# Kernel optimization log

Measured on AMD Instinct MI355X. Metric: run time of the kernel, lower is better.

The kernel has to match this reference:

```python
import jax, jax.numpy as jnp
import numpy as np

# dims
N, E, Z, C, NB = 8192, 131072, 10, 128, 8
R_MAX, P_CUT, AVG_NEIGH = 5.0, 5, 16.0
SH_DIM, N_L, N_LAYERS, MLP_H = 16, 4, 2, 16
# which l each of the 16 sh components belongs to
L_OF_M = jnp.array([0, 1, 1, 1, 2, 2, 2, 2, 2, 3, 3, 3, 3, 3, 3, 3])


def spherical_harmonics(u):
    """Real spherical harmonics up to l=3, e3nn 'component' normalization. u: [E,3] unit vectors."""
    x, y, z = u[:, 0], u[:, 1], u[:, 2]
    x2, y2, z2 = x * x, y * y, z * z
    s3, s5, s15 = np.sqrt(3.0), np.sqrt(5.0), np.sqrt(15.0)
    a33, a32, a31, a30 = 0.25 * np.sqrt(70.0), np.sqrt(105.0), 0.25 * np.sqrt(42.0), 0.5 * np.sqrt(7.0)
    Y = [jnp.ones_like(x),
         s3 * x, s3 * y, s3 * z,
         s15 * x * y, s15 * y * z, 0.5 * s5 * (3 * z2 - 1.0), s15 * x * z, 0.5 * s15 * (x2 - y2),
         a33 * y * (3 * x2 - y2), a32 * x * y * z, a31 * y * (5 * z2 - 1.0),
         a30 * z * (5 * z2 - 3.0), a31 * x * (5 * z2 - 1.0), 0.5 * a32 * z * (x2 - y2),
         a33 * x * (x2 - 3 * y2)]
    return jnp.stack(Y, axis=-1)  # [E,16]


def radial_embedding(r):
    """Bessel radial basis with smooth polynomial cutoff (p=5). r: [E] edge lengths."""
    x = r / R_MAX
    p = float(P_CUT)
    cut = (1.0 - 0.5 * (p + 1.0) * (p + 2.0) * x ** P_CUT
           + p * (p + 2.0) * x ** (P_CUT + 1) - 0.5 * p * (p + 1.0) * x ** (P_CUT + 2))
    cut = jnp.where(x < 1.0, cut, 0.0)
    n = jnp.arange(1, NB + 1, dtype=r.dtype)
    bessel = np.sqrt(2.0 / R_MAX) * jnp.sin(n[None, :] * jnp.pi * x[:, None]) / r[:, None]
    return bessel * cut[:, None]  # [E,8]


def _forward(positions, node_attrs, shifts, W_embed, W_up, R_w1, R_w2, R_w3,
             W_out, w_sc, w_prod, W_plin, w_ro0, ro_w1, ro_w2, edge_index):
    sender, receiver = edge_index[0], edge_index[1]
    vec = positions[receiver] - positions[sender] + shifts          # [E,3]
    lengths = jnp.linalg.norm(vec, axis=-1) + 1e-9                  # [E]
    sh = spherical_harmonics(vec / lengths[:, None])                # [E,16]
    edge_feats = radial_embedding(lengths)                          # [E,8]

    # node embedding: scalars into l=0 slot of [N,C,16]
    scalars = node_attrs @ W_embed                                  # [N,C]
    feats = jnp.zeros((N, C, SH_DIM), scalars.dtype).at[:, :, 0].set(scalars)

    outputs = []
    for L in range(N_LAYERS):
        # linear up (channel mixing, per irrep component)
        h = jnp.einsum('ncm,cd->ndm', feats, W_up[L])               # [N,C,16]
        # radial MLP -> per-edge, per-channel, per-l tensor-product weights
        r = jax.nn.silu(edge_feats @ R_w1[L])
        r = jax.nn.silu(r @ R_w2[L])
        w = (r @ R_w3[L]).reshape(E, C, N_L)                        # [E,C,4]
        w_m = jnp.take(w, L_OF_M, axis=2)                           # [E,C,16]
        # channel-wise tensor product: scalar node feat x SH, scatter to receiver
        msg = h[sender, :, 0][:, :, None] * w_m * sh[:, None, :]    # [E,C,16]
        agg = jax.ops.segment_sum(msg, receiver, num_segments=N) / AVG_NEIGH
        m = jnp.einsum('ncm,cd->ndm', agg, W_out[L])                # [N,C,16]
        # element-dependent skip connection
        sc = h * (node_attrs @ w_sc[L])[:, :, None]
        # product basis (correlation 3): element-weighted powers of scalar part
        s = m[:, :, 0]                                              # [N,C]
        coeff = jnp.einsum('nz,zck->nck', node_attrs, w_prod[L])    # [N,C,3]
        powers = jnp.stack([jnp.ones_like(s), s, s * s], axis=-1)   # [N,C,3]
        scale = jnp.sum(coeff * powers, axis=-1)                    # [N,C]
        feats = jnp.einsum('ncm,cd->ndm', m * scale[:, :, None], W_plin[L]) + sc
        if L == 0:
            outputs.append(feats[:, :, 0] @ w_ro0)                  # linear readout [N]
        else:
            outputs.append(jax.nn.silu(feats[:, :, 0] @ ro_w1) @ ro_w2)  # nonlinear readout [N]
    return outputs[0] + outputs[1]


def setup_inputs() -> dict:
    key = jax.random.key(0)
    ks = jax.random.split(key, 16)
    positions = jax.random.normal(ks[0], (N, 3), jnp.float32) * 1.5
    elems = jax.random.randint(ks[1], (N,), 0, Z)
    node_attrs = jax.nn.one_hot(elems, Z, dtype=jnp.float32)
    edge_index = jax.random.randint(ks[2], (2, E), 0, N)
    shifts = jnp.zeros((E, 3), jnp.float32)
    g = lambda k, sh, fan: jax.random.normal(k, sh, jnp.float32) / np.sqrt(fan)
    return {
        'positions': positions, 'node_attrs': node_attrs, 'shifts': shifts,
        'W_embed': g(ks[3], (Z, C), Z),
        'W_up': g(ks[4], (N_LAYERS, C, C), C),
        'R_w1': g(ks[5], (N_LAYERS, NB, 64), NB),
        'R_w2': g(ks[6], (N_LAYERS, 64, 64), 64),
        'R_w3': g(ks[7], (N_LAYERS, 64, C * N_L), 64),
        'W_out': g(ks[8], (N_LAYERS, C, C), C),
        'w_sc': g(ks[9], (N_LAYERS, Z, C), 1),
        'w_prod': g(ks[10], (N_LAYERS, Z, C, 3), 1) * 0.1,
        'W_plin': g(ks[11], (N_LAYERS, C, C), C),
        'w_ro0': g(ks[12], (C,), C),
        'ro_w1': g(ks[13], (C, MLP_H), C),
        'ro_w2': g(ks[14], (MLP_H,), MLP_H),
        'edge_index': edge_index,
    }


def reference(positions, node_attrs, shifts, W_embed, W_up, R_w1, R_w2, R_w3,
              W_out, w_sc, w_prod, W_plin, w_ro0, ro_w1, ro_w2, edge_index):
    return _forward(positions, node_attrs, shifts, W_embed, W_up, R_w1, R_w2, R_w3,
                    W_out, w_sc, w_prod, W_plin, w_ro0, ro_w1, ro_w2, edge_index)
```

## Files before the change

kernel.cpp:

```cpp
#include <hip/hip_runtime.h>
#include <math.h>

constexpr int kN = 8192;
constexpr int kE = 131072;
constexpr int NPB = 16;

typedef short bf16x8 __attribute__((ext_vector_type(8)));
typedef float f32x4 __attribute__((ext_vector_type(4)));
typedef unsigned short ushort_t;
typedef unsigned int uint_t;

__device__ __forceinline__ float silu_f(float x) { return x / (1.f + __expf(-x)); }

__device__ __forceinline__ ushort_t f2b(float f) {
  uint_t x = __float_as_uint(f);
  uint_t r = (x + 0x7fffu + ((x >> 16) & 1u)) >> 16;
  return (ushort_t)r;
}
__device__ __forceinline__ float b2f(ushort_t u) {
  return __uint_as_float(((uint_t)u) << 16);
}

__global__ __launch_bounds__(256) void zero_ints_kernel(int* __restrict__ a, int* __restrict__ b) {
  int i = blockIdx.x * 256 + threadIdx.x;
  if (i < kN) { a[i] = 0; b[i] = 0; }
}

__global__ __launch_bounds__(256) void elem_kernel(const float* __restrict__ attrs, int* __restrict__ elem) {
  int n = blockIdx.x * 256 + threadIdx.x;
  if (n >= kN) return;
  const float* a = attrs + (size_t)n * 10;
  int best = 0; float bv = a[0];
  #pragma unroll
  for (int z = 1; z < 10; ++z) { float v = a[z]; if (v > bv) { bv = v; best = z; } }
  elem[n] = best;
}

__global__ __launch_bounds__(256) void init_feats_kernel(const float* __restrict__ W_embed,
                                                         const int* __restrict__ elem,
                                                         ushort_t* __restrict__ F) {
  int i = blockIdx.x * 256 + threadIdx.x;
  int n = i >> 7, c = i & 127;
  F[(size_t)n * 2048 + c] = f2b(W_embed[(size_t)elem[n] * 128 + c]);
}

__global__ __launch_bounds__(256) void count_kernel(const int* __restrict__ ei, int* __restrict__ counts) {
  int e = blockIdx.x * 256 + threadIdx.x;
  if (e < kE) atomicAdd(&counts[ei[kE + e]], 1);
}

__global__ __launch_bounds__(1024) void scan_kernel(const int* __restrict__ counts, int* __restrict__ offs) {
  __shared__ int tmp[1024];
  int t = threadIdx.x;
  int loc[8]; int s = 0;
  #pragma unroll
  for (int i = 0; i < 8; ++i) { loc[i] = s; s += counts[t*8 + i]; }
  tmp[t] = s;
  __syncthreads();
  for (int d = 1; d < 1024; d <<= 1) {
    int v = (t >= d) ? tmp[t - d] : 0;
    __syncthreads();
    tmp[t] += v;
    __syncthreads();
  }
  int pre = (t == 0) ? 0 : tmp[t - 1];
  #pragma unroll
  for (int i = 0; i < 8; ++i) offs[t*8 + i] = pre + loc[i];
  if (t == 1023) offs[kN] = tmp[1023];
}

__global__ __launch_bounds__(256) void fill_kernel(const int* __restrict__ ei, const int* __restrict__ offs,
                                                   int* __restrict__ cursor, int* __restrict__ eids,
                                                   int* __restrict__ sends) {
  int e = blockIdx.x * 256 + threadIdx.x;
  if (e >= kE) return;
  int s = ei[e];
  int r = ei[kE + e];
  int pos = atomicAdd(&cursor[r], 1);
  eids[offs[r] + pos] = e;
  sends[offs[r] + pos] = s;
}

__global__ __launch_bounds__(256) void geom_kernel(const float* __restrict__ pos,
                                                   const float* __restrict__ shifts,
                                                   const int* __restrict__ ei,
                                                   const int* __restrict__ eids,
                                                   const int* __restrict__ sends,
                                                   float* __restrict__ sh,
                                                   float* __restrict__ rb) {
  int slot = blockIdx.x * 256 + threadIdx.x;
  if (slot >= kE) return;
  int e = eids[slot];
  int s = sends[slot];
  int r = ei[kE + e];
  float vx = pos[r*3+0] - pos[s*3+0] + shifts[(size_t)e*3+0];
  float vy = pos[r*3+1] - pos[s*3+1] + shifts[(size_t)e*3+1];
  float vz = pos[r*3+2] - pos[s*3+2] + shifts[(size_t)e*3+2];
  float len = sqrtf(vx*vx + vy*vy + vz*vz) + 1e-9f;
  float inv = 1.f / len;
  float x = vx*inv, y = vy*inv, z = vz*inv;
  float x2 = x*x, y2 = y*y, z2 = z*z;
  const float s3  = 1.7320508075688772f;
  const float s5  = 2.2360679774997896f;
  const float s15 = 3.8729833462074170f;
  const float a33 = 2.0916500663351889f;
  const float a32 = 10.246950765959598f;
  const float a31 = 1.6201851746019651f;
  const float a30 = 1.3228756555322954f;
  float4* shp = (float4*)(sh + (size_t)slot * 16);
  shp[0] = make_float4(1.f, s3*x, s3*y, s3*z);
  shp[1] = make_float4(s15*x*y, s15*y*z, 0.5f*s5*(3.f*z2 - 1.f), s15*x*z);
  shp[2] = make_float4(0.5f*s15*(x2 - y2), a33*y*(3.f*x2 - y2), a32*x*y*z, a31*y*(5.f*z2 - 1.f));
  shp[3] = make_float4(a30*z*(5.f*z2 - 3.f), a31*x*(5.f*z2 - 1.f), 0.5f*a32*z*(x2 - y2), a33*x*(x2 - 3.f*y2));
  float xr = len * 0.2f;
  float cut = 0.f;
  if (xr < 1.f) {
    float x5 = xr*xr*xr*xr*xr;
    cut = 1.f - 21.f*x5 + 35.f*x5*xr - 15.f*x5*xr*xr;
  }
  float pref = 0.63245553203367587f * cut * inv;
  const float PI = 3.14159265358979323846f;
  float theta = PI * xr;
  float sn, cs;
  __sincosf(theta, &sn, &cs);
  float twoc = 2.f * cs;
  float b[8];
  float s_prev = 0.f, s_cur = sn;
  b[0] = pref * s_cur;
  #pragma unroll
  for (int k = 1; k < 8; ++k) {
    float s_next = twoc * s_cur - s_prev;
    s_prev = s_cur; s_cur = s_next;
    b[k] = pref * s_cur;
  }
  float4* rbp = (float4*)(rb + (size_t)slot * 8);
  rbp[0] = make_float4(b[0], b[1], b[2], b[3]);
  rbp[1] = make_float4(b[4], b[5], b[6], b[7]);
}

__global__ __launch_bounds__(256) void radial_kernel(const float* __restrict__ rb,
                                                     const float* __restrict__ W1,
                                                     const float* __restrict__ W2,
                                                     ushort_t* __restrict__ r2) {
  __shared__ float rbs[128][8];
  __shared__ float W1s[8*64];
  __shared__ ushort_t B2s[64][72];
  __shared__ ushort_t r1s[128][72];
  const int tid = threadIdx.x;
  const size_t ebase = (size_t)blockIdx.x * 128;
  {
    int r = tid >> 1, q = tid & 1;
    *(float4*)&rbs[r][q*4] = *(const float4*)&rb[(ebase + r)*8 + q*4];
  }
  for (int i = tid; i < 512; i += 256) W1s[i] = W1[i];
  for (int i = tid; i < 4096; i += 256) {
    int k = i >> 6, col = i & 63;
    B2s[col][k] = f2b(W2[i]);
  }
  __syncthreads();
  {
    int col = tid & 63;
    int r0 = (tid >> 6) * 32;
    #pragma unroll 4
    for (int rr = 0; rr < 32; ++rr) {
      int row = r0 + rr;
      float v = 0.f;
      #pragma unroll
      for (int i = 0; i < 8; ++i) v = fmaf(rbs[row][i], W1s[i*64 + col], v);
      r1s[row][col] = f2b(silu_f(v));
    }
  }
  __syncthreads();
  const int lane = tid & 63, wv = tid >> 6;
  const int wr = wv * 32;
  const int fr = lane & 15, kg = (lane >> 4) * 8;
  f32x4 acc[2][4] = {};
  #pragma unroll
  for (int ks = 0; ks < 2; ++ks) {
    const int k0 = ks*32 + kg;
    bf16x8 af[2], bfr[4];
    #pragma unroll
    for (int i = 0; i < 2; ++i) af[i] = *(const bf16x8*)&r1s[wr + i*16 + fr][k0];
    #pragma unroll
    for (int j = 0; j < 4; ++j) bfr[j] = *(const bf16x8*)&B2s[j*16 + fr][k0];
    #pragma unroll
    for (int i = 0; i < 2; ++i)
      #pragma unroll
      for (int j = 0; j < 4; ++j)
        acc[i][j] = __builtin_amdgcn_mfma_f32_16x16x32_bf16(af[i], bfr[j], acc[i][j], 0, 0, 0);
  }
  __syncthreads();
  const int dcol = lane & 15, drow4 = (lane >> 4) * 4;
  #pragma unroll
  for (int i = 0; i < 2; ++i)
    #pragma unroll
    for (int j = 0; j < 4; ++j)
      #pragma unroll
      for (int r = 0; r < 4; ++r) {
        int row = wr + i*16 + drow4 + r;
        int col = j*16 + dcol;
        r1s[row][col] = f2b(silu_f(acc[i][j][r]));
      }
  __syncthreads();
  for (int idx = tid * 8; idx < 128*64; idx += 256*8) {
    int r = idx >> 6, k = idx & 63;
    *(int4*)&r2[(ebase + r)*64 + k] = *(const int4*)&r1s[r][k];
  }
}

__global__ __launch_bounds__(256) void transpose_w_kernel(const float* __restrict__ W, ushort_t* __restrict__ WT) {
  int i = blockIdx.x * 256 + threadIdx.x;
  int d = i >> 7, c = i & 127;
  WT[i] = f2b(W[c*128 + d]);
}

__global__ __launch_bounds__(256) void transpose_r3_kernel(const float* __restrict__ R3, ushort_t* __restrict__ R3T) {
  int i = blockIdx.x * 256 + threadIdx.x;
  int t = i >> 6, j = i & 63;
  int c = t & 127, l = t >> 7;
  R3T[i] = f2b(R3[j*512 + c*4 + l]);
}

template<bool SCALED, bool EPI, bool L0>
__global__ __launch_bounds__(256) void mgemm_kernel(
    const ushort_t* __restrict__ A, size_t aStride,
    const ushort_t* __restrict__ BT,
    ushort_t* __restrict__ O, size_t oStride,
    const float* __restrict__ scaleBuf,
    const ushort_t* __restrict__ Hbuf,
    const float* __restrict__ wscL,
    const int* __restrict__ elem)
{
  __shared__ ushort_t As[128][136];
  __shared__ ushort_t Bs[128][136];
  const int tid = threadIdx.x;
  const size_t rowbase = (size_t)blockIdx.x * 128;

  for (int idx = tid * 8; idx < 128 * 128; idx += 256 * 8) {
    int r = idx >> 7, k = idx & 127;
    *(int4*)&Bs[r][k] = *(const int4*)&BT[(size_t)r * 128 + k];
  }
  for (int idx = tid * 8; idx < 128 * 128; idx += 256 * 8) {
    int r = idx >> 7, k = idx & 127;
    size_t grow = rowbase + r;
    const ushort_t* ap = A + grow * aStride + k;
    if (SCALED) {
      const float* sp = scaleBuf + (grow >> 4) * 128 + k;
      uint_t u[4];
      #pragma unroll
      for (int q = 0; q < 4; ++q) {
        ushort_t lo = f2b(b2f(ap[2*q])   * sp[2*q]);
        ushort_t hi = f2b(b2f(ap[2*q+1]) * sp[2*q+1]);
        u[q] = (uint_t)lo | ((uint_t)hi << 16);
      }
      *(int4*)&As[r][k] = make_int4((int)u[0], (int)u[1], (int)u[2], (int)u[3]);
    } else {
      *(int4*)&As[r][k] = *(const int4*)ap;
    }
  }
  __syncthreads();

  const int lane = tid & 63, wv = tid >> 6;
  const int wr = (wv >> 1) * 64, wc = (wv & 1) * 64;
  const int fr = lane & 15;
  const int kg = (lane >> 4) * 8;
  f32x4 acc[4][4] = {};
  #pragma unroll
  for (int ks = 0; ks < 4; ++ks) {
    const int k0 = ks * 32 + kg;
    bf16x8 af[4], bfr[4];
    #pragma unroll
    for (int i = 0; i < 4; ++i) af[i]  = *(const bf16x8*)&As[wr + i*16 + fr][k0];
    #pragma unroll
    for (int j = 0; j < 4; ++j) bfr[j] = *(const bf16x8*)&Bs[wc + j*16 + fr][k0];
    #pragma unroll
    for (int i = 0; i < 4; ++i)
      #pragma unroll
      for (int j = 0; j < 4; ++j)
        acc[i][j] = __builtin_amdgcn_mfma_f32_16x16x32_bf16(af[i], bfr[j], acc[i][j], 0, 0, 0);
  }

  const int dcol = lane & 15, drow4 = (lane >> 4) * 4;
  #pragma unroll
  for (int i = 0; i < 4; ++i) {
    #pragma unroll
    for (int j = 0; j < 4; ++j) {
      int col = wc + j*16 + dcol;
      #pragma unroll
      for (int r = 0; r < 4; ++r) {
        int row = wr + i*16 + drow4 + r;
        size_t grow = rowbase + row;
        float v = acc[i][j][r];
        if (EPI) {
          if (!L0 || ((grow & 15) == 0)) {
            int ee = elem[grow >> 4];
            v += b2f(Hbuf[grow * 128 + col]) * wscL[(size_t)ee * 128 + col];
          }
        }
        O[grow * oStride + col] = f2b(v);
      }
    }
  }
}

__global__ __launch_bounds__(256, 2) void gather_kernel(
    const int* __restrict__ offs, const int* __restrict__ sends,
    const ushort_t* __restrict__ r2csr,
    const float* __restrict__ shcsr,
    const ushort_t* __restrict__ R3T,
    const ushort_t* __restrict__ H,
    ushort_t* __restrict__ AGG)
{
  __shared__ ushort_t r2s[2][32][68];
  __shared__ ushort_t h0s[2][32][68];
  __shared__ float    shs[2][32][17];
  const int tid = threadIdx.x;
  const int lane = tid & 63;
  const int l = tid >> 6;
  const int cbb = blockIdx.y * 64;
  const int mb = l * l, mc = 2 * l + 1;
  const int fr = lane & 15, g = lane >> 4, kg = g * 8;
  const int n0 = blockIdx.x * NPB;
  const int hslot = tid >> 3, hseg = tid & 7;
  const int s0i = tid, s1i = 256 + tid;

  bf16x8 bfrag[4][2];
  #pragma unroll
  for (int j = 0; j < 4; ++j)
    #pragma unroll
    for (int ks = 0; ks < 2; ++ks)
      bfrag[j][ks] = *(const bf16x8*)&R3T[(size_t)(l*128 + cbb + j*16 + fr) * 64 + ks*32 + kg];

  {
    int a0 = offs[n0], a1 = offs[n0 + 1];
    int4 h0v = make_int4(0,0,0,0), r2v = make_int4(0,0,0,0);
    float sv0 = 0.f, sv1 = 0.f;
    if (a0 + hslot < a1) {
      h0v = *(const int4*)&H[(size_t)sends[a0 + hslot] * 2048 + cbb + hseg * 8];
      r2v = *(const int4*)&r2csr[(size_t)(a0 + hslot) * 64 + hseg * 8];
    }
    if (a0 + (s0i >> 4) < a1) sv0 = shcsr[(size_t)(a0 + (s0i >> 4)) * 16 + (s0i & 15)];
    if (a0 + (s1i >> 4) < a1) sv1 = shcsr[(size_t)(a0 + (s1i >> 4)) * 16 + (s1i & 15)];
    *(int4*)&h0s[0][hslot][hseg * 8] = h0v;
    *(int4*)&r2s[0][hslot][hseg * 8] = r2v;
    shs[0][s0i >> 4][s0i & 15] = sv0;
    shs[0][s1i >> 4][s1i & 15] = sv1;
  }
  __syncthreads();

  int p = 0;
  for (int nn = n0; nn < n0 + NPB; ++nn) {
    const int e0n = offs[nn], e1n = offs[nn + 1];
    int4 h0n = make_int4(0,0,0,0), r2n = make_int4(0,0,0,0);
    float sn0 = 0.f, sn1 = 0.f;
    if (nn + 1 < n0 + NPB) {
      int a0 = offs[nn + 1], a1 = offs[nn + 2];
      if (a0 + hslot < a1) {
        h0n = *(const int4*)&H[(size_t)sends[a0 + hslot] * 2048 + cbb + hseg * 8];
        r2n = *(const int4*)&r2csr[(size_t)(a0 + hslot) * 64 + hseg * 8];
      }
      if (a0 + (s0i >> 4) < a1) sn0 = shcsr[(size_t)(a0 + (s0i >> 4)) * 16 + (s0i & 15)];
      if (a0 + (s1i >> 4) < a1) sn1 = shcsr[(size_t)(a0 + (s1i >> 4)) * 16 + (s1i & 15)];
    }

    float agg[7][4] = {};
    auto compute = [&](int pb) {
      f32x4 acc[2][4] = {};
      #pragma unroll
      for (int ks = 0; ks < 2; ++ks) {
        bf16x8 af[2];
        #pragma unroll
        for (int i = 0; i < 2; ++i) af[i] = *(const bf16x8*)&r2s[pb][i*16 + fr][ks*32 + kg];
        #pragma unroll
        for (int i = 0; i < 2; ++i)
          #pragma unroll
          for (int j = 0; j < 4; ++j)
            acc[i][j] = __builtin_amdgcn_mfma_f32_16x16x32_bf16(af[i], bfrag[j][ks], acc[i][j], 0, 0, 0);
      }
      #pragma unroll
      for (int i = 0; i < 2; ++i)
        #pragma unroll
        for (int r = 0; r < 4; ++r) {
          int slot = i*16 + g*4 + r;
          float shr[7];
          #pragma unroll
          for (int mi = 0; mi < 7; ++mi) shr[mi] = shs[pb][slot][mb + mi];
          #pragma unroll
          for (int j = 0; j < 4; ++j) {
            float wh = acc[i][j][r] * b2f(h0s[pb][slot][j*16 + fr]);
            #pragma unroll
            for (int mi = 0; mi < 7; ++mi)
              if (mi < mc) agg[mi][j] = fmaf(wh, shr[mi], agg[mi][j]);
          }
        }
    };
    compute(p);
    for (int base = e0n + 32; base < e1n; base += 32) {
      __syncthreads();
      int4 h0x = make_int4(0,0,0,0), r2x = make_int4(0,0,0,0);
      float sx0 = 0.f, sx1 = 0.f;
      if (base + hslot < e1n) {
        h0x = *(const int4*)&H[(size_t)sends[base + hslot] * 2048 + cbb + hseg * 8];
        r2x = *(const int4*)&r2csr[(size_t)(base + hslot) * 64 + hseg * 8];
      }
      if (base + (s0i >> 4) < e1n) sx0 = shcsr[(size_t)(base + (s0i >> 4)) * 16 + (s0i & 15)];
      if (base + (s1i >> 4) < e1n) sx1 = shcsr[(size_t)(base + (s1i >> 4)) * 16 + (s1i & 15)];
      *(int4*)&h0s[p][hslot][hseg * 8] = h0x;
      *(int4*)&r2s[p][hslot][hseg * 8] = r2x;
      shs[p][s0i >> 4][s0i & 15] = sx0;
      shs[p][s1i >> 4][s1i & 15] = sx1;
      __syncthreads();
      compute(p);
    }
    #pragma unroll
    for (int mi = 0; mi < 7; ++mi) {
      if (mi < mc) {
        #pragma unroll
        for (int j = 0; j < 4; ++j) {
          float v = agg[mi][j];
          v += __shfl_xor(v, 16, 64);
          v += __shfl_xor(v, 32, 64);
          if (lane < 16)
            AGG[(size_t)nn * 2048 + (mb + mi) * 128 + cbb + j * 16 + lane] = f2b(v * 0.0625f);
        }
      }
    }
    *(int4*)&h0s[p ^ 1][hslot][hseg * 8] = h0n;
    *(int4*)&r2s[p ^ 1][hslot][hseg * 8] = r2n;
    shs[p ^ 1][s0i >> 4][s0i & 15] = sn0;
    shs[p ^ 1][s1i >> 4][s1i & 15] = sn1;
    __syncthreads();
    p ^= 1;
  }
}

__global__ __launch_bounds__(256) void scale_kernel(const ushort_t* __restrict__ M,
                                                    const int* __restrict__ elem,
                                                    const float* __restrict__ wprodL,
                                                    float* __restrict__ scale) {
  int i = blockIdx.x * 256 + threadIdx.x;
  int n = i >> 7, c = i & 127;
  float s = b2f(M[(size_t)n * 2048 + c]);
  const float* co = wprodL + ((size_t)elem[n] * 128 + c) * 3;
  scale[i] = co[0] + s * (co[1] + s * co[2]);
}

__global__ __launch_bounds__(64) void readout_kernel(const ushort_t* __restrict__ F,
                                                     const float* __restrict__ ro0,
                                                     const float* __restrict__ ro1,
                                                     const float* __restrict__ ro2,
                                                     float* __restrict__ out, int layer) {
  int n = blockIdx.x; int t = threadIdx.x;
  const ushort_t* fr = F + (size_t)n * 2048;
  float f0 = b2f(fr[t]), f1 = b2f(fr[t + 64]);
  if (layer == 0) {
    float v = f0 * ro0[t] + f1 * ro0[t + 64];
    #pragma unroll
    for (int m = 32; m > 0; m >>= 1) v += __shfl_xor(v, m, 64);
    if (t == 0) out[n] = v;
  } else {
    float acc = 0.f;
    for (int h = 0; h < 16; ++h) {
      float p = f0 * ro1[t*16 + h] + f1 * ro1[(t + 64)*16 + h];
      #pragma unroll
      for (int m = 32; m > 0; m >>= 1) p += __shfl_xor(p, m, 64);
      acc = fmaf(silu_f(p), ro2[h], acc);
    }
    if (t == 0) out[n] += acc;
  }
}

extern "C" void kernel_launch(void* const* d_in, const int* in_sizes, int n_in,
                              void* d_out, int out_size, void* d_ws, size_t ws_size,
                              hipStream_t stream) {
  (void)in_sizes; (void)n_in; (void)out_size;
  const float* positions = (const float*)d_in[0];
  const float* node_attrs= (const float*)d_in[1];
  const float* shifts    = (const float*)d_in[2];
  const float* W_embed   = (const float*)d_in[3];
  const float* W_up      = (const float*)d_in[4];
  const float* R_w1      = (const float*)d_in[5];
  const float* R_w2      = (const float*)d_in[6];
  const float* R_w3      = (const float*)d_in[7];
  const float* W_out     = (const float*)d_in[8];
  const float* w_sc      = (const float*)d_in[9];
  const float* w_prod    = (const float*)d_in[10];
  const float* W_plin    = (const float*)d_in[11];
  const float* w_ro0     = (const float*)d_in[12];
  const float* ro_w1     = (const float*)d_in[13];
  const float* ro_w2     = (const float*)d_in[14];
  const int*   ei        = (const int*)d_in[15];
  float* out = (float*)d_out;

  char* ws_ptr = (char*)d_ws;
  size_t off = 0;
  auto alloc = [&](size_t nbytes) -> void* {
    void* p = ws_ptr + off;
    off += (nbytes + 255) & ~(size_t)255;
    return p;
  };
  const size_t PB = (size_t)kN * 16 * 128 * sizeof(ushort_t);
  ushort_t* P0    = (ushort_t*)alloc(PB);
  ushort_t* P1    = (ushort_t*)alloc(PB);
  ushort_t* P2    = (ushort_t*)alloc(PB);
  float* shcsr    = (float*)alloc((size_t)kE * 16 * 4);
  float* rbcsr    = (float*)alloc((size_t)kE * 8 * 4);
  ushort_t* r2csr = (ushort_t*)alloc((size_t)kE * 64 * 2);
  float* scaleb   = (float*)alloc((size_t)kN * 128 * 4);
  ushort_t* R3T0  = (ushort_t*)alloc(512 * 64 * 2);
  ushort_t* R3T1  = (ushort_t*)alloc(512 * 64 * 2);
  ushort_t* WTu0  = (ushort_t*)alloc(128 * 128 * 2);
  ushort_t* WTu1  = (ushort_t*)alloc(128 * 128 * 2);
  ushort_t* WTo0  = (ushort_t*)alloc(128 * 128 * 2);
  ushort_t* WTo1  = (ushort_t*)alloc(128 * 128 * 2);
  ushort_t* WTp0  = (ushort_t*)alloc(128 * 128 * 2);
  ushort_t* WTp1  = (ushort_t*)alloc(128 * 128 * 2);
  int* elemb  = (int*)alloc(kN * 4);
  int* counts = (int*)alloc(kN * 4);
  int* cursor = (int*)alloc(kN * 4);
  int* offsb  = (int*)alloc((kN + 1) * 4);
  int* eidsb  = (int*)alloc((size_t)kE * 4);
  int* sendsb = (int*)alloc((size_t)kE * 4);
  if (off > ws_size) return;

  zero_ints_kernel<<<kN/256, 256, 0, stream>>>(counts, cursor);
  elem_kernel<<<kN/256, 256, 0, stream>>>(node_attrs, elemb);
  init_feats_kernel<<<(kN*128)/256, 256, 0, stream>>>(W_embed, elemb, P0);
  count_kernel<<<kE/256, 256, 0, stream>>>(ei, counts);
  scan_kernel<<<1, 1024, 0, stream>>>(counts, offsb);
  fill_kernel<<<kE/256, 256, 0, stream>>>(ei, offsb, cursor, eidsb, sendsb);
  geom_kernel<<<kE/256, 256, 0, stream>>>(positions, shifts, ei, eidsb, sendsb, shcsr, rbcsr);
  transpose_w_kernel<<<64, 256, 0, stream>>>(W_up, WTu0);
  transpose_w_kernel<<<64, 256, 0, stream>>>(W_up + 16384, WTu1);
  transpose_w_kernel<<<64, 256, 0, stream>>>(W_out, WTo0);
  transpose_w_kernel<<<64, 256, 0, stream>>>(W_out + 16384, WTo1);
  transpose_w_kernel<<<64, 256, 0, stream>>>(W_plin, WTp0);
  transpose_w_kernel<<<64, 256, 0, stream>>>(W_plin + 16384, WTp1);
  transpose_r3_kernel<<<128, 256, 0, stream>>>(R_w3, R3T0);
  transpose_r3_kernel<<<128, 256, 0, stream>>>(R_w3 + 32768, R3T1);

  radial_kernel<<<kE/128, 256, 0, stream>>>(rbcsr, R_w1, R_w2, r2csr);
  mgemm_kernel<false,false,false><<<kN/128, 256, 0, stream>>>(
      P0, 2048, WTu0, P1, 2048, nullptr, nullptr, nullptr, nullptr);
  gather_kernel<<<dim3(kN/NPB, 2), 256, 0, stream>>>(offsb, sendsb, r2csr, shcsr, R3T0, P1, P2);
  mgemm_kernel<false,false,false><<<(kN*16)/128, 256, 0, stream>>>(
      P2, 128, WTo0, P0, 128, nullptr, nullptr, nullptr, nullptr);
  scale_kernel<<<(kN*128)/256, 256, 0, stream>>>(P0, elemb, w_prod, scaleb);
  mgemm_kernel<true,true,true><<<(kN*16)/128, 256, 0, stream>>>(
      P0, 128, WTp0, P2, 128, scaleb, P1, w_sc, elemb);
  readout_kernel<<<kN, 64, 0, stream>>>(P2, w_ro0, ro_w1, ro_w2, out, 0);

  radial_kernel<<<kE/128, 256, 0, stream>>>(rbcsr, R_w1 + 512, R_w2 + 4096, r2csr);
  mgemm_kernel<false,false,false><<<(kN*16)/128, 256, 0, stream>>>(
      P2, 128, WTu1, P1, 128, nullptr, nullptr, nullptr, nullptr);
  gather_kernel<<<dim3(kN/NPB, 2), 256, 0, stream>>>(offsb, sendsb, r2csr, shcsr, R3T1, P1, P0);
  mgemm_kernel<false,false,false><<<(kN*16)/128, 256, 0, stream>>>(
      P0, 128, WTo1, P2, 128, nullptr, nullptr, nullptr, nullptr);
  scale_kernel<<<(kN*128)/256, 256, 0, stream>>>(P2, elemb, w_prod + 3840, scaleb);
  mgemm_kernel<true,true,false><<<(kN*16)/128, 256, 0, stream>>>(
      P2, 128, WTp1, P0, 128, scaleb, P1, w_sc + 1280, elemb);
  readout_kernel<<<kN, 64, 0, stream>>>(P0, w_ro0, ro_w1, ro_w2, out, 1);
}
```

Measured before the change: 492.4 us.

## Process one node per block in gather kernel, dropping cross-node prefetch

```diff
diff --git a/kernel.cpp b/kernel.cpp
--- a/kernel.cpp
+++ b/kernel.cpp
@@ -3,7 +3,6 @@
 
 constexpr int kN = 8192;
 constexpr int kE = 131072;
-constexpr int NPB = 16;
 
 typedef short bf16x8 __attribute__((ext_vector_type(8)));
 typedef float f32x4 __attribute__((ext_vector_type(4)));
@@ -311,19 +310,21 @@
     const ushort_t* __restrict__ H,
     ushort_t* __restrict__ AGG)
 {
-  __shared__ ushort_t r2s[2][32][68];
-  __shared__ ushort_t h0s[2][32][68];
-  __shared__ float    shs[2][32][17];
+  __shared__ ushort_t r2s[32][68];
+  __shared__ ushort_t h0s[32][68];
+  __shared__ float    shs[32][17];
   const int tid = threadIdx.x;
   const int lane = tid & 63;
   const int l = tid >> 6;
   const int cbb = blockIdx.y * 64;
   const int mb = l * l, mc = 2 * l + 1;
   const int fr = lane & 15, g = lane >> 4, kg = g * 8;
-  const int n0 = blockIdx.x * NPB;
+  const int n = blockIdx.x;
   const int hslot = tid >> 3, hseg = tid & 7;
   const int s0i = tid, s1i = 256 + tid;
 
+  const int e0 = offs[n], e1 = offs[n + 1];
+
   bf16x8 bfrag[4][2];
   #pragma unroll
   for (int j = 0; j < 4; ++j)
@@ -331,106 +332,65 @@
     for (int ks = 0; ks < 2; ++ks)
       bfrag[j][ks] = *(const bf16x8*)&R3T[(size_t)(l*128 + cbb + j*16 + fr) * 64 + ks*32 + kg];
 
-  {
-    int a0 = offs[n0], a1 = offs[n0 + 1];
-    int4 h0v = make_int4(0,0,0,0), r2v = make_int4(0,0,0,0);
-    float sv0 = 0.f, sv1 = 0.f;
-    if (a0 + hslot < a1) {
-      h0v = *(const int4*)&H[(size_t)sends[a0 + hslot] * 2048 + cbb + hseg * 8];
-      r2v = *(const int4*)&r2csr[(size_t)(a0 + hslot) * 64 + hseg * 8];
-    }
-    if (a0 + (s0i >> 4) < a1) sv0 = shcsr[(size_t)(a0 + (s0i >> 4)) * 16 + (s0i & 15)];
-    if (a0 + (s1i >> 4) < a1) sv1 = shcsr[(size_t)(a0 + (s1i >> 4)) * 16 + (s1i & 15)];
-    *(int4*)&h0s[0][hslot][hseg * 8] = h0v;
-    *(int4*)&r2s[0][hslot][hseg * 8] = r2v;
-    shs[0][s0i >> 4][s0i & 15] = sv0;
-    shs[0][s1i >> 4][s1i & 15] = sv1;
-  }
-  __syncthreads();
-
-  int p = 0;
-  for (int nn = n0; nn < n0 + NPB; ++nn) {
-    const int e0n = offs[nn], e1n = offs[nn + 1];
-    int4 h0n = make_int4(0,0,0,0), r2n = make_int4(0,0,0,0);
-    float sn0 = 0.f, sn1 = 0.f;
-    if (nn + 1 < n0 + NPB) {
-      int a0 = offs[nn + 1], a1 = offs[nn + 2];
-      if (a0 + hslot < a1) {
-        h0n = *(const int4*)&H[(size_t)sends[a0 + hslot] * 2048 + cbb + hseg * 8];
-        r2n = *(const int4*)&r2csr[(size_t)(a0 + hslot) * 64 + hseg * 8];
+  float agg[7][4] = {};
+  for (int base = e0; base < e1; base += 32) {
+    if (base != e0) __syncthreads();
+    {
+      int4 h0v = make_int4(0,0,0,0), r2v = make_int4(0,0,0,0);
+      float sv0 = 0.f, sv1 = 0.f;
+      if (base + hslot < e1) {
+        h0v = *(const int4*)&H[(size_t)sends[base + hslot] * 2048 + cbb + hseg * 8];
+        r2v = *(const int4*)&r2csr[(size_t)(base + hslot) * 64 + hseg * 8];
       }
-      if (a0 + (s0i >> 4) < a1) sn0 = shcsr[(size_t)(a0 + (s0i >> 4)) * 16 + (s0i & 15)];
-      if (a0 + (s1i >> 4) < a1) sn1 = shcsr[(size_t)(a0 + (s1i >> 4)) * 16 + (s1i & 15)];
-    }
-
-    float agg[7][4] = {};
-    auto compute = [&](int pb) {
-      f32x4 acc[2][4] = {};
-      #pragma unroll
-      for (int ks = 0; ks < 2; ++ks) {
-        bf16x8 af[2];
-        #pragma unroll
-        for (int i = 0; i < 2; ++i) af[i] = *(const bf16x8*)&r2s[pb][i*16 + fr][ks*32 + kg];
-        #pragma unroll
-        for (int i = 0; i < 2; ++i)
-          #pragma unroll
-          for (int j = 0; j < 4; ++j)
-            acc[i][j] = __builtin_amdgcn_mfma_f32_16x16x32_bf16(af[i], bfrag[j][ks], acc[i][j], 0, 0, 0);
-      }
+      if (base + (s0i >> 4) < e1) sv0 = shcsr[(size_t)(base + (s0i >> 4)) * 16 + (s0i & 15)];
+      if (base + (s1i >> 4) < e1) sv1 = shcsr[(size_t)(base + (s1i >> 4)) * 16 + (s1i & 15)];
+      *(int4*)&h0s[hslot][hseg * 8] = h0v;
+      *(int4*)&r2s[hslot][hseg * 8] = r2v;
+      shs[s0i >> 4][s0i & 15] = sv0;
+      shs[s1i >> 4][s1i & 15] = sv1;
+    }
+    __syncthreads();
+    f32x4 acc[2][4] = {};
+    #pragma unroll
+    for (int ks = 0; ks < 2; ++ks) {
+      bf16x8 af[2];
+      #pragma unroll
+      for (int i = 0; i < 2; ++i) af[i] = *(const bf16x8*)&r2s[i*16 + fr][ks*32 + kg];
       #pragma unroll
       for (int i = 0; i < 2; ++i)
         #pragma unroll
-        for (int r = 0; r < 4; ++r) {
-          int slot = i*16 + g*4 + r;
-          float shr[7];
-          #pragma unroll
-          for (int mi = 0; mi < 7; ++mi) shr[mi] = shs[pb][slot][mb + mi];
-          #pragma unroll
-          for (int j = 0; j < 4; ++j) {
-            float wh = acc[i][j][r] * b2f(h0s[pb][slot][j*16 + fr]);
-            #pragma unroll
-            for (int mi = 0; mi < 7; ++mi)
-              if (mi < mc) agg[mi][j] = fmaf(wh, shr[mi], agg[mi][j]);
-          }
-        }
-    };
-    compute(p);
-    for (int base = e0n + 32; base < e1n; base += 32) {
-      __syncthreads();
-      int4 h0x = make_int4(0,0,0,0), r2x = make_int4(0,0,0,0);
-      float sx0 = 0.f, sx1 = 0.f;
-      if (base + hslot < e1n) {
-        h0x = *(const int4*)&H[(size_t)sends[base + hslot] * 2048 + cbb + hseg * 8];
-        r2x = *(const int4*)&r2csr[(size_t)(base + hslot) * 64 + hseg * 8];
-      }
-      if (base + (s0i >> 4) < e1n) sx0 = shcsr[(size_t)(base + (s0i >> 4)) * 16 + (s0i & 15)];
-      if (base + (s1i >> 4) < e1n) sx1 = shcsr[(size_t)(base + (s1i >> 4)) * 16 + (s1i & 15)];
-      *(int4*)&h0s[p][hslot][hseg * 8] = h0x;
-      *(int4*)&r2s[p][hslot][hseg * 8] = r2x;
-      shs[p][s0i >> 4][s0i & 15] = sx0;
-      shs[p][s1i >> 4][s1i & 15] = sx1;
-      __syncthreads();
-      compute(p);
-    }
-    #pragma unroll
-    for (int mi = 0; mi < 7; ++mi) {
-      if (mi < mc) {
+        for (int j = 0; j < 4; ++j)
+          acc[i][j] = __builtin_amdgcn_mfma_f32_16x16x32_bf16(af[i], bfrag[j][ks], acc[i][j], 0, 0, 0);
+    }
+    #pragma unroll
+    for (int i = 0; i < 2; ++i)
+      #pragma unroll
+      for (int r = 0; r < 4; ++r) {
+        int slot = i*16 + g*4 + r;
+        float shr[7];
+        #pragma unroll
+        for (int mi = 0; mi < 7; ++mi) shr[mi] = shs[slot][mb + mi];
         #pragma unroll
         for (int j = 0; j < 4; ++j) {
-          float v = agg[mi][j];
-          v += __shfl_xor(v, 16, 64);
-          v += __shfl_xor(v, 32, 64);
-          if (lane < 16)
-            AGG[(size_t)nn * 2048 + (mb + mi) * 128 + cbb + j * 16 + lane] = f2b(v * 0.0625f);
+          float wh = acc[i][j][r] * b2f(h0s[slot][j*16 + fr]);
+          #pragma unroll
+          for (int mi = 0; mi < 7; ++mi)
+            if (mi < mc) agg[mi][j] = fmaf(wh, shr[mi], agg[mi][j]);
         }
       }
-    }
-    *(int4*)&h0s[p ^ 1][hslot][hseg * 8] = h0n;
-    *(int4*)&r2s[p ^ 1][hslot][hseg * 8] = r2n;
-    shs[p ^ 1][s0i >> 4][s0i & 15] = sn0;
-    shs[p ^ 1][s1i >> 4][s1i & 15] = sn1;
-    __syncthreads();
-    p ^= 1;
+  }
+  #pragma unroll
+  for (int mi = 0; mi < 7; ++mi) {
+    if (mi < mc) {
+      #pragma unroll
+      for (int j = 0; j < 4; ++j) {
+        float v = agg[mi][j];
+        v += __shfl_xor(v, 16, 64);
+        v += __shfl_xor(v, 32, 64);
+        if (lane < 16)
+          AGG[(size_t)n * 2048 + (mb + mi) * 128 + cbb + j * 16 + lane] = f2b(v * 0.0625f);
+      }
+    }
   }
 }
 
@@ -542,7 +502,7 @@
   radial_kernel<<<kE/128, 256, 0, stream>>>(rbcsr, R_w1, R_w2, r2csr);
   mgemm_kernel<false,false,false><<<kN/128, 256, 0, stream>>>(
       P0, 2048, WTu0, P1, 2048, nullptr, nullptr, nullptr, nullptr);
-  gather_kernel<<<dim3(kN/NPB, 2), 256, 0, stream>>>(offsb, sendsb, r2csr, shcsr, R3T0, P1, P2);
+  gather_kernel<<<dim3(kN, 2), 256, 0, stream>>>(offsb, sendsb, r2csr, shcsr, R3T0, P1, P2);
   mgemm_kernel<false,false,false><<<(kN*16)/128, 256, 0, stream>>>(
       P2, 128, WTo0, P0, 128, nullptr, nullptr, nullptr, nullptr);
   scale_kernel<<<(kN*128)/256, 256, 0, stream>>>(P0, elemb, w_prod, scaleb);
@@ -553,7 +513,7 @@
   radial_kernel<<<kE/128, 256, 0, stream>>>(rbcsr, R_w1 + 512, R_w2 + 4096, r2csr);
   mgemm_kernel<false,false,false><<<(kN*16)/128, 256, 0, stream>>>(
       P2, 128, WTu1, P1, 128, nullptr, nullptr, nullptr, nullptr);
-  gather_kernel<<<dim3(kN/NPB, 2), 256, 0, stream>>>(offsb, sendsb, r2csr, shcsr, R3T1, P1, P0);
+  gather_kernel<<<dim3(kN, 2), 256, 0, stream>>>(offsb, sendsb, r2csr, shcsr, R3T1, P1, P0);
   mgemm_kernel<false,false,false><<<(kN*16)/128, 256, 0, stream>>>(
       P0, 128, WTo1, P2, 128, nullptr, nullptr, nullptr, nullptr);
   scale_kernel<<<(kN*128)/256, 256, 0, stream>>>(P2, elemb, w_prod + 3840, scaleb);
```

Result: slower. 579.5 us (+17.7%).
